# Kernel tuning notes

Measured on AMD Instinct MI355X. Metric: run time of the kernel, lower is better.

Reference implementation:

```python
import jax, jax.numpy as jnp
import numpy as np

N, E, K, D, H, ED = 10000, 200000, 16, 64, 4, 16


def setup_inputs() -> dict:
    key = jax.random.key(0)
    ks = iter(jax.random.split(key, 64))
    def nrm(shape, s=1.0):
        return jax.random.normal(next(ks), shape, dtype=jnp.float32) * s
    def lin(fi, fo):
        return nrm((fi, fo), 1.0 / np.sqrt(fi))
    inp = {}
    inp['h'] = nrm((N, D))
    inp['coord'] = nrm((N, 3))
    nv = nrm((N, 3)); inp['nvecs'] = nv / (jnp.linalg.norm(nv, axis=-1, keepdims=True) + 1e-8)
    inp['edge_attr'] = nrm((E, ED))
    inp['node_attr'] = nrm((N, D))
    inp['init_coord'] = nrm((N, 3))
    iv = nrm((N, 3)); inp['init_nvecs'] = iv / (jnp.linalg.norm(iv, axis=-1, keepdims=True) + 1e-8)
    # Ch_Pos_GCL params (Linear weights stored as (in, out))
    inp['ch_W1'] = lin(4 * D + ED, D); inp['ch_b1'] = jnp.zeros((D,))
    inp['ch_W2'] = lin(D, D);          inp['ch_b2'] = jnp.zeros((D,))
    inp['pos_W1'] = lin(2, D);         inp['pos_b1'] = jnp.zeros((D,))
    inp['pos_W2'] = lin(D, D);         inp['pos_b2'] = jnp.zeros((D,))
    inp['sh_W'] = lin(D, D);           inp['sh_b'] = jnp.zeros((D,))
    inp['att_W'] = lin(D, 1);          inp['att_b'] = jnp.zeros((1,))
    # Tri_Att_GCL per-head params stacked over heads
    inp['Wq'] = nrm((H, D, D), 1.0 / np.sqrt(D))
    inp['Wk'] = nrm((H, D, D), 1.0 / np.sqrt(D))
    inp['Wv'] = nrm((H, D, D), 1.0 / np.sqrt(D))
    inp['Wb'] = nrm((H, D), 1.0 / np.sqrt(D))
    inp['Wg'] = nrm((H, D, D), 1.0 / np.sqrt(D))
    inp['bg'] = jnp.zeros((H, D))
    inp['out_W'] = lin(H * D, D);      inp['out_b'] = jnp.zeros((D,))
    # phi MLPs
    inp['phiu_W1'] = lin(D, D); inp['phiu_b1'] = jnp.zeros((D,)); inp['phiu_W2'] = lin(D, 1); inp['phiu_b2'] = jnp.zeros((1,))
    inp['phix_W1'] = lin(D, D); inp['phix_b1'] = jnp.zeros((D,)); inp['phix_W2'] = lin(D, 1); inp['phix_b2'] = jnp.zeros((1,))
    inp['phin_W1'] = lin(D, D); inp['phin_b1'] = jnp.zeros((D,)); inp['phin_W2'] = lin(D, 1); inp['phin_b2'] = jnp.zeros((1,))
    inp['phih_W1'] = lin(2 * D + D, D); inp['phih_b1'] = jnp.zeros((D,))
    inp['phih_W2'] = lin(D, D);         inp['phih_b2'] = jnp.zeros((D,))
    # int inputs
    inp['edges'] = jax.random.randint(next(ks), (2, E), 0, N)
    idx = jax.random.randint(next(ks), (E, 2, K), 0, E)
    pad = jax.random.uniform(next(ks), (E, 1, K)) < 0.1
    inp['klist'] = jnp.where(pad, -1, idx)
    return inp


def reference(h, coord, nvecs, edge_attr, node_attr, init_coord, init_nvecs,
              ch_W1, ch_b1, ch_W2, ch_b2, pos_W1, pos_b1, pos_W2, pos_b2,
              sh_W, sh_b, att_W, att_b, Wq, Wk, Wv, Wb, Wg, bg, out_W, out_b,
              phiu_W1, phiu_b1, phiu_W2, phiu_b2, phix_W1, phix_b1, phix_W2, phix_b2,
              phin_W1, phin_b1, phin_W2, phin_b2, phih_W1, phih_b1, phih_W2, phih_b2,
              edges, klist):
    silu = jax.nn.silu
    row, col = edges[0], edges[1]
    # --- Ch_Pos_GCL ---
    diff = coord[row] - coord[col]                      # (E, 3)
    radial = jnp.sum(diff * diff, axis=1, keepdims=True)
    coord_diff = diff / (jnp.sqrt(radial) + 1e-8)
    nprod = jnp.sum(nvecs[row] * nvecs[col], axis=-1, keepdims=True)
    chem_in = jnp.concatenate([h[row], h[col], node_attr[row], node_attr[col], edge_attr], axis=1)
    chem = silu(silu(chem_in @ ch_W1 + ch_b1) @ ch_W2 + ch_b2)          # (E, D)
    pos = silu(silu(jnp.concatenate([nprod, radial], axis=1) @ pos_W1 + pos_b1) @ pos_W2 + pos_b2)
    out = silu(chem @ sh_W + sh_b) * pos
    z = out * jax.nn.sigmoid(out @ att_W + att_b)                        # (E, D)
    # --- Tri_Att_GCL (k-neighbor triangle attention) ---
    idx_i2k, idx_j2k = klist[:, 0], klist[:, 1]          # (E, K)
    fmask = (idx_i2k != -1).astype(z.dtype)              # redundant slots -> 0
    scale = 1.0 / np.sqrt(D)
    head_outs = []
    for hd in range(H):
        q = z @ Wq[hd]; k = z @ Wk[hd]; v = z @ Wv[hd]
        b = z @ Wb[hd]                                   # (E,)
        g = jax.nn.sigmoid(z @ Wg[hd] + bg[hd])
        tri_k = k[idx_i2k] * fmask[..., None]            # (E, K, D)
        tri_v = v[idx_i2k] * fmask[..., None]
        tri_b = b[idx_j2k] * fmask                       # (E, K)
        alpha = jax.nn.softmax(scale * jnp.einsum('ed,ekd->ek', q, tri_k) + tri_b, axis=1)
        head_outs.append(g * jnp.einsum('ek,ekd->ed', alpha, tri_v))
    m = jnp.concatenate(head_outs, axis=-1) @ out_W + out_b             # (E, D)
    # --- aggregation / updates ---
    def mlp2(x, W1, b1, W2, b2):
        return silu(x @ W1 + b1) @ W2 + b2
    def seg_mean(data, ids, n):
        s = jax.ops.segment_sum(data, ids, num_segments=n)
        c = jax.ops.segment_sum(jnp.ones_like(data), ids, num_segments=n)
        return s / jnp.clip(c, 1.0)
    n_nodes = coord.shape[0]
    phi_u = mlp2(chem, phiu_W1, phiu_b1, phiu_W2, phiu_b2)              # (E, 1)
    phi_x = mlp2(pos, phix_W1, phix_b1, phix_W2, phix_b2)
    phi_n = mlp2(pos, phin_W1, phin_b1, phin_W2, phin_b2)
    x_agg = seg_mean(coord_diff * (phi_u * phi_x), row, n_nodes)
    coord_new = 0.2 * init_coord + 0.8 * coord + x_agg
    n_agg = seg_mean(nvecs[col] * (phi_u * phi_n), row, n_nodes)
    nv = 0.2 * init_nvecs + 0.8 * nvecs + n_agg
    nv = nv / (jnp.linalg.norm(nv, axis=-1, keepdims=True) + 1e-8)
    m_agg = seg_mean(m, row, n_nodes)
    h_new = 0.2 * h + 0.8 * mlp2(jnp.concatenate([h, node_attr, m_agg], axis=-1), phih_W1, phih_b1, phih_W2, phih_b2)
    return (h_new, coord_new, nv)
```

## Files before the change

kernel.cpp:

```cpp
#include <hip/hip_runtime.h>

typedef unsigned short u16;
typedef unsigned int u32;
typedef __attribute__((ext_vector_type(8))) short s16x8;
typedef __attribute__((ext_vector_type(4))) float f32x4;

#define NN 10000
#define EE 200000
#define ES ((size_t)EE * 64)
#define NTILE 3125

#define DEVI __device__ __forceinline__

DEVI float us2f(u16 u) {
    union { u32 i; float f; } v; v.i = ((u32)u) << 16; return v.f;
}
DEVI u16 f2bu(float f) {
    union { float f; u32 i; } v; v.f = f;
    u32 x = v.i;
    return (u16)((x + 0x7fffu + ((x >> 16) & 1u)) >> 16);
}
DEVI float siluf(float x) { return x / (1.f + __expf(-x)); }
DEVI float sigmf(float x) { return 1.f / (1.f + __expf(-x)); }
DEVI float waveSum(float v) {
#pragma unroll
    for (int o = 32; o; o >>= 1) v += __shfl_xor(v, o);
    return v;
}
DEVI float quadSum(float v) {
#pragma unroll
    for (int o = 1; o < 16; o <<= 1) v += __shfl_xor(v, o);
    return v;
}

__device__ u16 g_hb[(size_t)NN * 64];
__device__ u16 g_nab[(size_t)NN * 64];
__device__ u16 g_eab[(size_t)EE * 16];
__device__ u16 g_t1[ES];
__device__ u16 g_z16[ES];
__device__ u16 g_t4[4][ES];
__device__ __align__(16) u16 g_Mt[4][4608];
__device__ __align__(16) u16 g_wpre[12][4608];
__device__ __align__(16) u16 g_wmA[6][4608];
__device__ __align__(16) u16 g_w1t[64 * 296];
__device__ float g_b4[(size_t)EE * 4];
__device__ float g_nr[EE];
__device__ float g_rad[EE];
__device__ float g_cdl[EE * 3];
__device__ int g_degi[NN];
__device__ int g_fill[NN];
__device__ int g_roff[NN + 1];
__device__ int g_eid[EE];
__device__ float g_me[(size_t)EE * 64];
__device__ float g_xe[EE * 3];
__device__ float g_ne[EE * 3];
__device__ float g_mavg[(size_t)NN * 64];

__global__ __launch_bounds__(256) void k_zero()
{
    int t = blockIdx.x * 256 + threadIdx.x;
    if (t < NN) { g_degi[t] = 0; g_fill[t] = 0; }
}

__global__ __launch_bounds__(256) void k_prep(
    const float* __restrict__ Wq, const float* __restrict__ Wk,
    const float* __restrict__ h, const float* __restrict__ na, const float* __restrict__ ea,
    const float* __restrict__ coord, const float* __restrict__ nvecs,
    const float* __restrict__ Wv, const float* __restrict__ Wg, const float* __restrict__ oW,
    const float* __restrict__ posW2, const float* __restrict__ chW2, const float* __restrict__ shW,
    const float* __restrict__ uW1, const float* __restrict__ xW1, const float* __restrict__ nW1,
    const float* __restrict__ chemW1,
    const int* __restrict__ edges)
{
    int t = blockIdx.x * 256 + threadIdx.x;
    if (t < 16384) {
        int hd = t >> 12, rem = t & 4095, k = rem >> 6, n = rem & 63;
        const float* wq = Wq + (size_t)hd * 4096 + k * 64;
        const float* wk = Wk + (size_t)hd * 4096 + n * 64;
        float acc = 0.f;
        for (int d = 0; d < 64; d++) acc += wq[d] * wk[d];
        int off = n * 72 + k;
        g_Mt[hd][off] = f2bu(acc);
        g_wpre[hd * 3 + 0][off] = f2bu(Wv[t]);
        g_wpre[hd * 3 + 1][off] = f2bu(oW[t]);
        g_wpre[hd * 3 + 2][off] = f2bu(Wg[t]);
    }
    int nt = gridDim.x * 256;
    for (int i = t; i < 6 * 4096; i += nt) {
        int a = i >> 12, rem = i & 4095, k = rem >> 6, n = rem & 63;
        const float* s;
        if (a == 0) s = posW2;
        else if (a == 1) s = chW2;
        else if (a == 2) s = shW;
        else if (a == 3) s = uW1;
        else if (a == 4) s = xW1;
        else s = nW1;
        g_wmA[a][n * 72 + k] = f2bu(s[rem]);
    }
    for (int i = t; i < 64 * 296; i += nt) {
        int n = i / 296, k = i - n * 296;
        g_w1t[i] = (k < 272) ? f2bu(chemW1[k * 64 + n]) : (u16)0;
    }
    for (int i = t; i < NN * 64; i += nt) { g_hb[i] = f2bu(h[i]); g_nab[i] = f2bu(na[i]); }
    for (size_t i = t; i < (size_t)EE * 16; i += nt) g_eab[i] = f2bu(ea[i]);
    for (int e = t; e < EE; e += nt) {
        int r = edges[e], c = edges[EE + e];
        atomicAdd(&g_degi[r], 1);
        float d0 = coord[r * 3 + 0] - coord[c * 3 + 0];
        float d1 = coord[r * 3 + 1] - coord[c * 3 + 1];
        float d2 = coord[r * 3 + 2] - coord[c * 3 + 2];
        float radial = d0 * d0 + d1 * d1 + d2 * d2;
        float np = nvecs[r * 3 + 0] * nvecs[c * 3 + 0]
                 + nvecs[r * 3 + 1] * nvecs[c * 3 + 1]
                 + nvecs[r * 3 + 2] * nvecs[c * 3 + 2];
        float rinv = 1.f / (sqrtf(radial) + 1e-8f);
        g_cdl[e * 3 + 0] = d0 * rinv;
        g_cdl[e * 3 + 1] = d1 * rinv;
        g_cdl[e * 3 + 2] = d2 * rinv;
        g_nr[e] = np;
        g_rad[e] = radial;
    }
}

__global__ __launch_bounds__(256) void k_scan()
{
    __shared__ int ls[256];
    int tid = threadIdx.x;
    int basei = tid * 40;
    int loc[40];
    int cnt = 0;
#pragma unroll
    for (int i = 0; i < 40; i++) {
        int idx = basei + i;
        int v = (idx < NN) ? g_degi[idx] : 0;
        loc[i] = cnt; cnt += v;
    }
    ls[tid] = cnt;
    __syncthreads();
    int off = 0;
    for (int i = 0; i < tid; i++) off += ls[i];
#pragma unroll
    for (int i = 0; i < 40; i++) {
        int idx = basei + i;
        if (idx < NN) g_roff[idx] = off + loc[i];
    }
    if (tid == 255) g_roff[NN] = off + cnt;
}

__global__ __launch_bounds__(256) void k_fill(const int* __restrict__ edges)
{
    int e = blockIdx.x * 256 + threadIdx.x;
    if (e < EE) {
        int r = edges[e];
        int slot = atomicAdd(&g_fill[r], 1);
        g_eid[g_roff[r] + slot] = e;
    }
}

__global__ __launch_bounds__(256) void k_chem1(
    const int* __restrict__ edges, const float* __restrict__ b1)
{
    __shared__ __align__(16) u16 sBT[64 * 296];
    int tid = threadIdx.x;
    {
        u32* d = (u32*)sBT; const u32* s = (const u32*)g_w1t;
        for (int i = tid; i < 9472; i += 256) d[i] = s[i];
    }
    __syncthreads();
    int lane = tid & 63, q = lane >> 4, ln = lane & 15, w = tid >> 6;
    int base = blockIdx.x * 2;
    int nt2 = (base + 1 < NTILE) ? 2 : 1;
    for (int t2 = 0; t2 < nt2; t2++) {
        int m0 = (base + t2) * 64 + w * 16;
        int e = m0 + ln;
        int r_ = edges[e], c_ = edges[EE + e];
        f32x4 acc[4];
#pragma unroll
        for (int t = 0; t < 4; t++) acc[t] = (f32x4){0.f, 0.f, 0.f, 0.f};
#pragma unroll
        for (int k0 = 0; k0 < 9; k0++) {
            int k = k0 * 32 + q * 8;
            const u16* p = nullptr;
            if (k < 64)       p = g_hb  + (size_t)r_ * 64 + k;
            else if (k < 128) p = g_hb  + (size_t)c_ * 64 + (k - 64);
            else if (k < 192) p = g_nab + (size_t)r_ * 64 + (k - 128);
            else if (k < 256) p = g_nab + (size_t)c_ * 64 + (k - 192);
            else if (k < 272) p = g_eab + (size_t)e * 16 + (k - 256);
            s16x8 af = p ? *(const s16x8*)p : (s16x8){0, 0, 0, 0, 0, 0, 0, 0};
#pragma unroll
            for (int t = 0; t < 4; t++) {
                s16x8 bf = *(const s16x8*)(&sBT[(t * 16 + ln) * 296 + k0 * 32 + q * 8]);
                acc[t] = __builtin_amdgcn_mfma_f32_16x16x32_bf16(af, bf, acc[t], 0, 0, 0);
            }
        }
#pragma unroll
        for (int t = 0; t < 4; t++) {
            float bv = b1[t * 16 + ln];
#pragma unroll
            for (int r = 0; r < 4; r++)
                g_t1[(size_t)(m0 + q * 4 + r) * 64 + t * 16 + ln] = f2bu(siluf(acc[t][r] + bv));
        }
    }
}

DEVI void stageP(u16* dst, const u16* src, int tid) {
    u32* d = (u32*)dst; const u32* s = (const u32*)src;
    for (int i = tid; i < 2304; i += 256) d[i] = s[i];
}

__global__ __launch_bounds__(256) void k_megaAB(
    const float* __restrict__ chb2,
    const float* __restrict__ pW1, const float* __restrict__ pb1,
    const float* __restrict__ posb2,
    const float* __restrict__ shb,
    const float* __restrict__ attW, const float* __restrict__ attb,
    const float* __restrict__ Wb,
    const float* __restrict__ ub1, const float* __restrict__ uW2, const float* __restrict__ ub2,
    const float* __restrict__ xb1, const float* __restrict__ xW2, const float* __restrict__ xb2,
    const float* __restrict__ nb1, const float* __restrict__ nW2, const float* __restrict__ nb2,
    const int* __restrict__ edges, const float* __restrict__ nvecs)
{
    __shared__ __align__(16) u16 sW0[64 * 72], sW1b[64 * 72], sW2b[64 * 72];
    __shared__ u16 T[4][16 * 72];
    __shared__ float sWB[256], sATT[64], sPW1[128], sPB1[64];
    int tid = threadIdx.x;
    stageP(sW0, g_wmA[0], tid); stageP(sW1b, g_wmA[1], tid); stageP(sW2b, g_wmA[2], tid);
    sWB[tid] = Wb[tid];
    if (tid < 128) sPW1[tid] = pW1[tid];
    if (tid < 64) { sATT[tid] = attW[tid]; sPB1[tid] = pb1[tid]; }
    __syncthreads();
    int lane = tid & 63, q = lane >> 4, ln = lane & 15, w = tid >> 6;
    int m0 = blockIdx.x * 64 + w * 16;
    float np_ = g_nr[m0 + ln], rad_ = g_rad[m0 + ln];
    s16x8 p1f0, p1f1;
#pragma unroll
    for (int j = 0; j < 8; j++) {
        int k = q * 8 + j;
        p1f0[j] = (short)f2bu(siluf(sPB1[k] + np_ * sPW1[k] + rad_ * sPW1[64 + k]));
        k += 32;
        p1f1[j] = (short)f2bu(siluf(sPB1[k] + np_ * sPW1[k] + rad_ * sPW1[64 + k]));
    }
    f32x4 pacc[4];
#pragma unroll
    for (int t = 0; t < 4; t++) {
        f32x4 a = (f32x4){0,0,0,0};
        a = __builtin_amdgcn_mfma_f32_16x16x32_bf16(p1f0, *(const s16x8*)(&sW0[(t * 16 + ln) * 72 + q * 8]), a, 0, 0, 0);
        a = __builtin_amdgcn_mfma_f32_16x16x32_bf16(p1f1, *(const s16x8*)(&sW0[(t * 16 + ln) * 72 + 32 + q * 8]), a, 0, 0, 0);
        pacc[t] = a;
    }
    float posD[4][4];
#pragma unroll
    for (int t = 0; t < 4; t++) {
        float pb = posb2[t * 16 + ln];
#pragma unroll
        for (int r = 0; r < 4; r++) posD[t][r] = siluf(pacc[t][r] + pb);
    }
    f32x4 cacc[4];
#pragma unroll
    for (int t = 0; t < 4; t++) cacc[t] = (f32x4){0,0,0,0};
    {
        const u16* ar = g_t1 + (size_t)(m0 + ln) * 64;
#pragma unroll
        for (int k0 = 0; k0 < 2; k0++) {
            s16x8 af = *(const s16x8*)(ar + k0 * 32 + q * 8);
#pragma unroll
            for (int t = 0; t < 4; t++) {
                s16x8 bf = *(const s16x8*)(&sW1b[(t * 16 + ln) * 72 + k0 * 32 + q * 8]);
                cacc[t] = __builtin_amdgcn_mfma_f32_16x16x32_bf16(af, bf, cacc[t], 0, 0, 0);
            }
        }
    }
#pragma unroll
    for (int t = 0; t < 4; t++) {
        float cb = chb2[t * 16 + ln];
#pragma unroll
        for (int r = 0; r < 4; r++)
            T[w][(q * 4 + r) * 72 + t * 16 + ln] = f2bu(siluf(cacc[t][r] + cb));
    }
    asm volatile("s_waitcnt lgkmcnt(0)" ::: "memory");
    s16x8 ca0 = *(const s16x8*)(&T[w][ln * 72 + q * 8]);
    s16x8 ca1 = *(const s16x8*)(&T[w][ln * 72 + 32 + q * 8]);
    f32x4 sacc[4];
#pragma unroll
    for (int t = 0; t < 4; t++) {
        f32x4 a = (f32x4){0,0,0,0};
        a = __builtin_amdgcn_mfma_f32_16x16x32_bf16(ca0, *(const s16x8*)(&sW2b[(t * 16 + ln) * 72 + q * 8]), a, 0, 0, 0);
        a = __builtin_amdgcn_mfma_f32_16x16x32_bf16(ca1, *(const s16x8*)(&sW2b[(t * 16 + ln) * 72 + 32 + q * 8]), a, 0, 0, 0);
        sacc[t] = a;
    }
    float zv[4][4];
    float part4[4] = {0.f, 0.f, 0.f, 0.f};
#pragma unroll
    for (int t = 0; t < 4; t++) {
        float sb = shb[t * 16 + ln];
        float aw = sATT[t * 16 + ln];
#pragma unroll
        for (int r = 0; r < 4; r++) {
            float o = siluf(sacc[t][r] + sb) * posD[t][r];
            zv[t][r] = o;
            part4[r] += o * aw;
        }
    }
    float ab = attb[0];
#pragma unroll
    for (int r = 0; r < 4; r++) {
        float sg = sigmf(quadSum(part4[r]) + ab);
        size_t row = m0 + q * 4 + r;
#pragma unroll
        for (int t = 0; t < 4; t++) {
            float z = zv[t][r] * sg;
            zv[t][r] = z;
            g_z16[row * 64 + t * 16 + ln] = f2bu(z);
        }
    }
#pragma unroll
    for (int hd = 0; hd < 4; hd++) {
#pragma unroll
        for (int r = 0; r < 4; r++) {
            float p = 0.f;
#pragma unroll
            for (int t = 0; t < 4; t++) p += zv[t][r] * sWB[hd * 64 + t * 16 + ln];
            p = quadSum(p);
            if (ln == hd) g_b4[(size_t)(m0 + q * 4 + r) * 4 + hd] = p;
        }
    }
#pragma unroll
    for (int t = 0; t < 4; t++)
#pragma unroll
        for (int r = 0; r < 4; r++)
            T[w][(q * 4 + r) * 72 + t * 16 + ln] = f2bu(posD[t][r]);
    asm volatile("s_waitcnt lgkmcnt(0)" ::: "memory");
    s16x8 pa0 = *(const s16x8*)(&T[w][ln * 72 + q * 8]);
    s16x8 pa1 = *(const s16x8*)(&T[w][ln * 72 + 32 + q * 8]);
    __syncthreads();
    stageP(sW0, g_wmA[3], tid); stageP(sW1b, g_wmA[4], tid); stageP(sW2b, g_wmA[5], tid);
    __syncthreads();
    f32x4 uacc[4];
#pragma unroll
    for (int t = 0; t < 4; t++) {
        f32x4 a = (f32x4){0,0,0,0};
        a = __builtin_amdgcn_mfma_f32_16x16x32_bf16(ca0, *(const s16x8*)(&sW0[(t * 16 + ln) * 72 + q * 8]), a, 0, 0, 0);
        a = __builtin_amdgcn_mfma_f32_16x16x32_bf16(ca1, *(const s16x8*)(&sW0[(t * 16 + ln) * 72 + 32 + q * 8]), a, 0, 0, 0);
        uacc[t] = a;
    }
    float up[4] = {0.f, 0.f, 0.f, 0.f};
#pragma unroll
    for (int t = 0; t < 4; t++) {
        float ub = ub1[t * 16 + ln];
        float w2 = uW2[t * 16 + ln];
#pragma unroll
        for (int r = 0; r < 4; r++) up[r] += siluf(uacc[t][r] + ub) * w2;
    }
    float ub2v = ub2[0];
    float pu[4];
#pragma unroll
    for (int r = 0; r < 4; r++) pu[r] = quadSum(up[r]) + ub2v;
    f32x4 xacc[4], nacc[4];
#pragma unroll
    for (int t = 0; t < 4; t++) {
        f32x4 a = (f32x4){0,0,0,0}, b = (f32x4){0,0,0,0};
        a = __builtin_amdgcn_mfma_f32_16x16x32_bf16(pa0, *(const s16x8*)(&sW1b[(t * 16 + ln) * 72 + q * 8]), a, 0, 0, 0);
        a = __builtin_amdgcn_mfma_f32_16x16x32_bf16(pa1, *(const s16x8*)(&sW1b[(t * 16 + ln) * 72 + 32 + q * 8]), a, 0, 0, 0);
        b = __builtin_amdgcn_mfma_f32_16x16x32_bf16(pa0, *(const s16x8*)(&sW2b[(t * 16 + ln) * 72 + q * 8]), b, 0, 0, 0);
        b = __builtin_amdgcn_mfma_f32_16x16x32_bf16(pa1, *(const s16x8*)(&sW2b[(t * 16 + ln) * 72 + 32 + q * 8]), b, 0, 0, 0);
        xacc[t] = a; nacc[t] = b;
    }
    float xp[4] = {0,0,0,0}, npv[4] = {0,0,0,0};
#pragma unroll
    for (int t = 0; t < 4; t++) {
        float xb = xb1[t * 16 + ln], nb = nb1[t * 16 + ln];
        float xw = xW2[t * 16 + ln], nw = nW2[t * 16 + ln];
#pragma unroll
        for (int r = 0; r < 4; r++) {
            xp[r] += siluf(xacc[t][r] + xb) * xw;
            npv[r] += siluf(nacc[t][r] + nb) * nw;
        }
    }
    float xb2v = xb2[0], nb2v = nb2[0];
#pragma unroll
    for (int r = 0; r < 4; r++) {
        float phix = quadSum(xp[r]) + xb2v;
        float phin = quadSum(npv[r]) + nb2v;
        int row = m0 + q * 4 + r;
        float tx = pu[r] * phix, tn = pu[r] * phin;
        int cc = edges[EE + row];
        if (ln < 3) {
            g_xe[row * 3 + ln] = g_cdl[row * 3 + ln] * tx;
            g_ne[row * 3 + ln] = nvecs[cc * 3 + ln] * tn;
        }
    }
}

struct STG { s16x8 za0, za1, qb0, qb1; f32x4 bv; };

__global__ __launch_bounds__(64) void k_attn2(const int* __restrict__ klist)
{
    __shared__ u16 sQP[16][256];
    __shared__ u16 zT[16 * 72];
    __shared__ __align__(16) float sA[4][16];
    int lane = threadIdx.x & 63, q = lane >> 4, ln = lane & 15;
    int m0 = blockIdx.x * 16;
    u16* zw = zT;

    {
        const u16* zr = g_z16 + (size_t)(m0 + ln) * 64;
        s16x8 af0 = *(const s16x8*)(zr + q * 8);
        s16x8 af1 = *(const s16x8*)(zr + 32 + q * 8);
#pragma unroll
        for (int hd = 0; hd < 4; hd++) {
            f32x4 aM[4];
#pragma unroll
            for (int t = 0; t < 4; t++) {
                f32x4 a = (f32x4){0,0,0,0};
                a = __builtin_amdgcn_mfma_f32_16x16x32_bf16(af0, *(const s16x8*)(&g_Mt[hd][(t * 16 + ln) * 72 + q * 8]), a, 0, 0, 0);
                a = __builtin_amdgcn_mfma_f32_16x16x32_bf16(af1, *(const s16x8*)(&g_Mt[hd][(t * 16 + ln) * 72 + 32 + q * 8]), a, 0, 0, 0);
                aM[t] = a;
            }
#pragma unroll
            for (int t = 0; t < 4; t++)
#pragma unroll
                for (int r = 0; r < 4; r++)
                    sQP[q * 4 + r][hd * 64 + t * 16 + ln] = f2bu(aM[t][r]);
        }
    }
    asm volatile("s_waitcnt lgkmcnt(0)" ::: "memory");

    auto ldkl = [&](int j) -> int {
        return (lane < 32) ? klist[(size_t)(m0 + j) * 32 + lane] : -1;
    };
    auto stage = [&](int kv, int j) -> STG {
        STG s;
        s.za0 = (s16x8){0,0,0,0,0,0,0,0}; s.za1 = (s16x8){0,0,0,0,0,0,0,0};
        s.qb0 = (s16x8){0,0,0,0,0,0,0,0}; s.qb1 = (s16x8){0,0,0,0,0,0,0,0};
        int ij = __shfl(kv, ln);
        if (ij >= 0) {
            const u16* zr = g_z16 + (size_t)ij * 64;
            s.za0 = *(const s16x8*)(zr + q * 8);
            s.za1 = *(const s16x8*)(zr + 32 + q * 8);
        }
        if (ln < 4) {
            s.qb0 = *(const s16x8*)(&sQP[j][ln * 64 + q * 8]);
            s.qb1 = *(const s16x8*)(&sQP[j][ln * 64 + 32 + q * 8]);
        }
        s.bv = (f32x4){0.f, 0.f, 0.f, 0.f};
#pragma unroll
        for (int r = 0; r < 4; r++) {
            int ijj = __shfl(kv, q * 4 + r);
            int jj = __shfl(kv, 16 + q * 4 + r);
            s.bv[r] = (ijj >= 0 && ln < 4) ? g_b4[(size_t)jj * 4 + ln] : 0.f;
        }
        return s;
    };

    int kvA = ldkl(0), kvB = ldkl(1), kvC = ldkl(2);
    STG s0 = stage(kvA, 0);
    STG s1 = stage(kvB, 1);
#pragma unroll 1
    for (int j = 0; j < 16; j++) {
        int kvD = (j + 3 < 16) ? ldkl(j + 3) : -1;
        STG s2;
        if (j + 2 < 16) s2 = stage(kvC, j + 2);
        else {
            s2.za0 = (s16x8){0,0,0,0,0,0,0,0}; s2.za1 = s2.za0;
            s2.qb0 = s2.za0; s2.qb1 = s2.za0;
            s2.bv = (f32x4){0.f, 0.f, 0.f, 0.f};
        }
        f32x4 sc = (f32x4){0.f, 0.f, 0.f, 0.f};
        sc = __builtin_amdgcn_mfma_f32_16x16x32_bf16(s0.za0, s0.qb0, sc, 0, 0, 0);
        sc = __builtin_amdgcn_mfma_f32_16x16x32_bf16(s0.za1, s0.qb1, sc, 0, 0, 0);
        *(s16x8*)(&zw[ln * 72 + q * 8]) = s0.za0;
        *(s16x8*)(&zw[ln * 72 + 32 + q * 8]) = s0.za1;
        float s[4];
#pragma unroll
        for (int r = 0; r < 4; r++) s[r] = 0.125f * sc[r] + s0.bv[r];
        float mx = fmaxf(fmaxf(s[0], s[1]), fmaxf(s[2], s[3]));
        mx = fmaxf(mx, __shfl_xor(mx, 16));
        mx = fmaxf(mx, __shfl_xor(mx, 32));
        float ex[4], ps = 0.f;
#pragma unroll
        for (int r = 0; r < 4; r++) { ex[r] = __expf(s[r] - mx); ps += ex[r]; }
        ps += __shfl_xor(ps, 16);
        ps += __shfl_xor(ps, 32);
        float inv = 1.f / ps;
        if (ln < 4)
            *(f32x4*)&sA[ln][q * 4] = (f32x4){ex[0] * inv, ex[1] * inv, ex[2] * inv, ex[3] * inv};
        asm volatile("s_waitcnt lgkmcnt(0)" ::: "memory");
        float t0 = 0.f, t1 = 0.f, t2 = 0.f, t3 = 0.f;
#pragma unroll
        for (int j4 = 0; j4 < 4; j4++) {
            f32x4 a0 = *(const f32x4*)&sA[0][j4 * 4];
            f32x4 a1 = *(const f32x4*)&sA[1][j4 * 4];
            f32x4 a2 = *(const f32x4*)&sA[2][j4 * 4];
            f32x4 a3 = *(const f32x4*)&sA[3][j4 * 4];
#pragma unroll
            for (int r = 0; r < 4; r++) {
                float zz = us2f(zw[(j4 * 4 + r) * 72 + lane]);
                t0 += a0[r] * zz; t1 += a1[r] * zz; t2 += a2[r] * zz; t3 += a3[r] * zz;
            }
        }
        size_t ob = (size_t)(m0 + j) * 64 + lane;
        g_t4[0][ob] = f2bu(t0);
        g_t4[1][ob] = f2bu(t1);
        g_t4[2][ob] = f2bu(t2);
        g_t4[3][ob] = f2bu(t3);
        kvA = kvB; kvB = kvC; kvC = kvD;
        s0 = s1; s1 = s2;
    }
}

__global__ __launch_bounds__(256) void k_us(
    const float* __restrict__ bg, const int* __restrict__ edges)
{
    __shared__ u16 sU[4][16 * 72];
    int tid = threadIdx.x;
    int lane = tid & 63, q = lane >> 4, ln = lane & 15, w = tid >> 6;
    int m0 = blockIdx.x * 64 + w * 16;
    const u16* zr = g_z16 + (size_t)(m0 + ln) * 64;
    s16x8 za[2];
    za[0] = *(const s16x8*)(zr + q * 8);
    za[1] = *(const s16x8*)(zr + 32 + q * 8);
    f32x4 macc[4];
#pragma unroll
    for (int t = 0; t < 4; t++) macc[t] = (f32x4){0,0,0,0};
    for (int hd = 0; hd < 4; hd++) {
        const u16* wV = g_wpre[hd * 3 + 0];
        const u16* wO = g_wpre[hd * 3 + 1];
        const u16* wG = g_wpre[hd * 3 + 2];
        f32x4 vacc[4], gacc[4];
#pragma unroll
        for (int t = 0; t < 4; t++) { vacc[t] = (f32x4){0,0,0,0}; gacc[t] = (f32x4){0,0,0,0}; }
        const u16* ar = &g_t4[hd][(size_t)(m0 + ln) * 64];
#pragma unroll
        for (int k0 = 0; k0 < 2; k0++) {
            s16x8 af = *(const s16x8*)(ar + k0 * 32 + q * 8);
#pragma unroll
            for (int t = 0; t < 4; t++) {
                vacc[t] = __builtin_amdgcn_mfma_f32_16x16x32_bf16(
                    af, *(const s16x8*)(&wV[(t * 16 + ln) * 72 + k0 * 32 + q * 8]), vacc[t], 0, 0, 0);
                gacc[t] = __builtin_amdgcn_mfma_f32_16x16x32_bf16(
                    za[k0], *(const s16x8*)(&wG[(t * 16 + ln) * 72 + k0 * 32 + q * 8]), gacc[t], 0, 0, 0);
            }
        }
#pragma unroll
        for (int t = 0; t < 4; t++) {
            float bb = bg[hd * 64 + t * 16 + ln];
#pragma unroll
            for (int r = 0; r < 4; r++) {
                float u = vacc[t][r] * sigmf(gacc[t][r] + bb);
                sU[w][(q * 4 + r) * 72 + t * 16 + ln] = f2bu(u);
            }
        }
        asm volatile("s_waitcnt lgkmcnt(0)" ::: "memory");
#pragma unroll
        for (int k0 = 0; k0 < 2; k0++) {
            s16x8 af = *(const s16x8*)(&sU[w][ln * 72 + k0 * 32 + q * 8]);
#pragma unroll
            for (int t = 0; t < 4; t++) {
                macc[t] = __builtin_amdgcn_mfma_f32_16x16x32_bf16(
                    af, *(const s16x8*)(&wO[(t * 16 + ln) * 72 + k0 * 32 + q * 8]), macc[t], 0, 0, 0);
            }
        }
        asm volatile("s_waitcnt lgkmcnt(0)" ::: "memory");
    }
#pragma unroll
    for (int r = 0; r < 4; r++) {
        size_t dst = (size_t)(m0 + q * 4 + r) * 64;
#pragma unroll
        for (int t = 0; t < 4; t++) g_me[dst + t * 16 + ln] = macc[t][r];
    }
}

__global__ __launch_bounds__(256) void k_agg(
    const float* __restrict__ coord, const float* __restrict__ nvecs,
    const float* __restrict__ icoord, const float* __restrict__ invecs,
    const float* __restrict__ ob, float* __restrict__ out)
{
    int tid = threadIdx.x;
    int lane = tid & 63;
    int n = blockIdx.x * 4 + (tid >> 6);
    if (n >= NN) return;
    int r0 = g_roff[n], r1 = g_roff[n + 1];
    int deg = r1 - r0;
    float msA = 0.f, msB = 0.f, msC = 0.f, msD = 0.f;
    float xs0 = 0.f, xs1 = 0.f, xs2 = 0.f, ns0 = 0.f, ns1 = 0.f, ns2 = 0.f;
    for (int base = r0; base < r1; base += 64) {
        int idx = base + lane;
        int e_l = (idx < r1) ? g_eid[idx] : -1;
        int cnt = min(64, r1 - base);
        int j = 0;
        for (; j + 3 < cnt; j += 4) {
            int ea = __shfl(e_l, j), eb = __shfl(e_l, j + 1);
            int ec = __shfl(e_l, j + 2), ed = __shfl(e_l, j + 3);
            msA += g_me[(size_t)ea * 64 + lane];
            msB += g_me[(size_t)eb * 64 + lane];
            msC += g_me[(size_t)ec * 64 + lane];
            msD += g_me[(size_t)ed * 64 + lane];
        }
        for (; j < cnt; j++) {
            int ea = __shfl(e_l, j);
            msA += g_me[(size_t)ea * 64 + lane];
        }
        if (e_l >= 0) {
            xs0 += g_xe[e_l * 3 + 0]; xs1 += g_xe[e_l * 3 + 1]; xs2 += g_xe[e_l * 3 + 2];
            ns0 += g_ne[e_l * 3 + 0]; ns1 += g_ne[e_l * 3 + 1]; ns2 += g_ne[e_l * 3 + 2];
        }
    }
    xs0 = waveSum(xs0); xs1 = waveSum(xs1); xs2 = waveSum(xs2);
    ns0 = waveSum(ns0); ns1 = waveSum(ns1); ns2 = waveSum(ns2);
    float rinv = 1.f / fmaxf((float)deg, 1.f);
    float obv = (deg > 0) ? ob[lane] : 0.f;
    g_mavg[(size_t)n * 64 + lane] = (msA + msB + msC + msD) * rinv + obv;
    if (lane == 0) {
        size_t coff = (size_t)NN * 64;
        size_t noff = coff + (size_t)NN * 3;
        float xs[3] = {xs0, xs1, xs2}, ns[3] = {ns0, ns1, ns2};
        float nl[3];
#pragma unroll
        for (int c = 0; c < 3; c++) {
            out[coff + n * 3 + c] = 0.2f * icoord[n * 3 + c] + 0.8f * coord[n * 3 + c] + xs[c] * rinv;
            nl[c] = 0.2f * invecs[n * 3 + c] + 0.8f * nvecs[n * 3 + c] + ns[c] * rinv;
        }
        float nn2 = sqrtf(nl[0] * nl[0] + nl[1] * nl[1] + nl[2] * nl[2]) + 1e-8f;
#pragma unroll
        for (int c = 0; c < 3; c++) out[noff + n * 3 + c] = nl[c] / nn2;
    }
}

__global__ __launch_bounds__(256) void k_node(
    const float* __restrict__ h, const float* __restrict__ na,
    const float* __restrict__ W1, const float* __restrict__ b1,
    const float* __restrict__ W2, const float* __restrict__ b2,
    float* __restrict__ out)
{
    __shared__ u16 sW1T[64 * 200];
    __shared__ u16 sW2T[64 * 72];
    __shared__ u16 sA[64 * 200];
    __shared__ u16 sT[64 * 72];
    __shared__ float sb2v[64];
    int tid = threadIdx.x;
    int m0 = blockIdx.x * 64;
    for (int i = tid; i < 64 * 192; i += 256) {
        int n = i / 192, k = i - n * 192;
        sW1T[n * 200 + k] = f2bu(W1[k * 64 + n]);
    }
    for (int i = tid; i < 4096; i += 256) {
        int k = i >> 6, n = i & 63;
        sW2T[n * 72 + k] = f2bu(W2[i]);
    }
    if (tid < 64) sb2v[tid] = b2[tid];
    for (int i = tid; i < 4096; i += 256) {
        int row = i >> 6, d = i & 63;
        int n = m0 + row; if (n >= NN) n = NN - 1;
        sA[row * 200 + d] = f2bu(h[(size_t)n * 64 + d]);
        sA[row * 200 + 64 + d] = f2bu(na[(size_t)n * 64 + d]);
        sA[row * 200 + 128 + d] = f2bu(g_mavg[(size_t)n * 64 + d]);
    }
    __syncthreads();
    int lane = tid & 63, q = lane >> 4, ln = lane & 15, w = tid >> 6;
    f32x4 acc[4];
#pragma unroll
    for (int t = 0; t < 4; t++) acc[t] = (f32x4){0.f, 0.f, 0.f, 0.f};
#pragma unroll
    for (int k0 = 0; k0 < 6; k0++) {
        s16x8 af = *(const s16x8*)(&sA[(w * 16 + ln) * 200 + k0 * 32 + q * 8]);
#pragma unroll
        for (int t = 0; t < 4; t++) {
            s16x8 bf = *(const s16x8*)(&sW1T[(t * 16 + ln) * 200 + k0 * 32 + q * 8]);
            acc[t] = __builtin_amdgcn_mfma_f32_16x16x32_bf16(af, bf, acc[t], 0, 0, 0);
        }
    }
#pragma unroll
    for (int t = 0; t < 4; t++) {
        float bv = b1[t * 16 + ln];
#pragma unroll
        for (int r = 0; r < 4; r++)
            sT[(w * 16 + q * 4 + r) * 72 + t * 16 + ln] = f2bu(siluf(acc[t][r] + bv));
    }
    asm volatile("s_waitcnt lgkmcnt(0)" ::: "memory");
    f32x4 acc2[4];
#pragma unroll
    for (int t = 0; t < 4; t++) acc2[t] = (f32x4){0.f, 0.f, 0.f, 0.f};
#pragma unroll
    for (int k0 = 0; k0 < 2; k0++) {
        s16x8 af = *(const s16x8*)(&sT[(w * 16 + ln) * 72 + k0 * 32 + q * 8]);
#pragma unroll
        for (int t = 0; t < 4; t++) {
            s16x8 bf = *(const s16x8*)(&sW2T[(t * 16 + ln) * 72 + k0 * 32 + q * 8]);
            acc2[t] = __builtin_amdgcn_mfma_f32_16x16x32_bf16(af, bf, acc2[t], 0, 0, 0);
        }
    }
#pragma unroll
    for (int r = 0; r < 4; r++) {
        int n = m0 + w * 16 + q * 4 + r;
        if (n < NN) {
#pragma unroll
            for (int t = 0; t < 4; t++) {
                int d = t * 16 + ln;
                out[(size_t)n * 64 + d] = 0.2f * h[(size_t)n * 64 + d] + 0.8f * (acc2[t][r] + sb2v[d]);
            }
        }
    }
}

extern "C" void kernel_launch(void* const* d_in, const int* in_sizes, int n_in,
                              void* d_out, int out_size, void* d_ws, size_t ws_size,
                              hipStream_t stream)
{
    const int* edges = (const int*)d_in[43];
    const int* klist = (const int*)d_in[44];
    auto F = [&](int i) { return (const float*)d_in[i]; };

    k_zero<<<40, 256, 0, stream>>>();
    k_prep<<<512, 256, 0, stream>>>(F(19), F(20), F(0), F(4), F(3), F(1), F(2),
                                    F(21), F(23), F(25),
                                    F(13), F(9), F(15), F(27), F(31), F(35), F(7),
                                    edges);
    k_scan<<<1, 256, 0, stream>>>();
    k_fill<<<782, 256, 0, stream>>>(edges);
    k_chem1<<<1563, 256, 0, stream>>>(edges, F(8));
    k_megaAB<<<3125, 256, 0, stream>>>(F(10), F(11), F(12), F(14),
                                       F(16), F(17), F(18), F(22),
                                       F(28), F(29), F(30),
                                       F(32), F(33), F(34),
                                       F(36), F(37), F(38),
                                       edges, F(2));
    k_attn2<<<12500, 64, 0, stream>>>(klist);
    k_us<<<3125, 256, 0, stream>>>(F(24), edges);
    k_agg<<<2500, 256, 0, stream>>>(F(1), F(2), F(5), F(6), F(26), (float*)d_out);
    k_node<<<157, 256, 0, stream>>>(F(0), F(4), F(39), F(40), F(41), F(42), (float*)d_out);
}
```

Measured before the change: 642.3 us.

## Fuse gated value/output projection into attention kernel, keep head outputs in LDS

The per-head attention results are now kept in shared memory inside the attention kernel, and the gated V projection plus output projection run in the same kernel instead of a separate launch. This removes writing and re-reading four E×64 bf16 intermediate arrays through global memory, plus one kernel launch. In exchange the attention kernel uses more LDS and registers, which may lower occupancy, and the projection now runs as 64-thread blocks instead of 256-thread blocks.

```diff
diff --git a/kernel.cpp b/kernel.cpp
--- a/kernel.cpp
+++ b/kernel.cpp
@@ -38,7 +38,6 @@
 __device__ u16 g_eab[(size_t)EE * 16];
 __device__ u16 g_t1[ES];
 __device__ u16 g_z16[ES];
-__device__ u16 g_t4[4][ES];
 __device__ __align__(16) u16 g_Mt[4][4608];
 __device__ __align__(16) u16 g_wpre[12][4608];
 __device__ __align__(16) u16 g_wmA[6][4608];
@@ -393,27 +392,29 @@
 
 struct STG { s16x8 za0, za1, qb0, qb1; f32x4 bv; };
 
-__global__ __launch_bounds__(64) void k_attn2(const int* __restrict__ klist)
-{
-    __shared__ u16 sQP[16][256];
-    __shared__ u16 zT[16 * 72];
+__global__ __launch_bounds__(64) void k_attn2(const int* __restrict__ klist,
+                                              const float* __restrict__ bg)
+{
+    __shared__ __align__(16) u16 sQP[16][256];
+    __shared__ __align__(16) u16 zT[16 * 72];
+    __shared__ __align__(16) u16 sT4[4][16 * 72];
     __shared__ __align__(16) float sA[4][16];
     int lane = threadIdx.x & 63, q = lane >> 4, ln = lane & 15;
     int m0 = blockIdx.x * 16;
     u16* zw = zT;
 
+    const u16* zro = g_z16 + (size_t)(m0 + ln) * 64;
+    s16x8 zaf0 = *(const s16x8*)(zro + q * 8);
+    s16x8 zaf1 = *(const s16x8*)(zro + 32 + q * 8);
     {
-        const u16* zr = g_z16 + (size_t)(m0 + ln) * 64;
-        s16x8 af0 = *(const s16x8*)(zr + q * 8);
-        s16x8 af1 = *(const s16x8*)(zr + 32 + q * 8);
 #pragma unroll
         for (int hd = 0; hd < 4; hd++) {
             f32x4 aM[4];
 #pragma unroll
             for (int t = 0; t < 4; t++) {
                 f32x4 a = (f32x4){0,0,0,0};
-                a = __builtin_amdgcn_mfma_f32_16x16x32_bf16(af0, *(const s16x8*)(&g_Mt[hd][(t * 16 + ln) * 72 + q * 8]), a, 0, 0, 0);
-                a = __builtin_amdgcn_mfma_f32_16x16x32_bf16(af1, *(const s16x8*)(&g_Mt[hd][(t * 16 + ln) * 72 + 32 + q * 8]), a, 0, 0, 0);
+                a = __builtin_amdgcn_mfma_f32_16x16x32_bf16(zaf0, *(const s16x8*)(&g_Mt[hd][(t * 16 + ln) * 72 + q * 8]), a, 0, 0, 0);
+                a = __builtin_amdgcn_mfma_f32_16x16x32_bf16(zaf1, *(const s16x8*)(&g_Mt[hd][(t * 16 + ln) * 72 + 32 + q * 8]), a, 0, 0, 0);
                 aM[t] = a;
             }
 #pragma unroll
@@ -498,27 +499,16 @@
                 t0 += a0[r] * zz; t1 += a1[r] * zz; t2 += a2[r] * zz; t3 += a3[r] * zz;
             }
         }
-        size_t ob = (size_t)(m0 + j) * 64 + lane;
-        g_t4[0][ob] = f2bu(t0);
-        g_t4[1][ob] = f2bu(t1);
-        g_t4[2][ob] = f2bu(t2);
-        g_t4[3][ob] = f2bu(t3);
+        sT4[0][j * 72 + lane] = f2bu(t0);
+        sT4[1][j * 72 + lane] = f2bu(t1);
+        sT4[2][j * 72 + lane] = f2bu(t2);
+        sT4[3][j * 72 + lane] = f2bu(t3);
         kvA = kvB; kvB = kvC; kvC = kvD;
         s0 = s1; s1 = s2;
     }
-}
-
-__global__ __launch_bounds__(256) void k_us(
-    const float* __restrict__ bg, const int* __restrict__ edges)
-{
-    __shared__ u16 sU[4][16 * 72];
-    int tid = threadIdx.x;
-    int lane = tid & 63, q = lane >> 4, ln = lane & 15, w = tid >> 6;
-    int m0 = blockIdx.x * 64 + w * 16;
-    const u16* zr = g_z16 + (size_t)(m0 + ln) * 64;
-    s16x8 za[2];
-    za[0] = *(const s16x8*)(zr + q * 8);
-    za[1] = *(const s16x8*)(zr + 32 + q * 8);
+
+    asm volatile("s_waitcnt lgkmcnt(0)" ::: "memory");
+    u16* uT = &sQP[0][0];
     f32x4 macc[4];
 #pragma unroll
     for (int t = 0; t < 4; t++) macc[t] = (f32x4){0,0,0,0};
@@ -529,16 +519,16 @@
         f32x4 vacc[4], gacc[4];
 #pragma unroll
         for (int t = 0; t < 4; t++) { vacc[t] = (f32x4){0,0,0,0}; gacc[t] = (f32x4){0,0,0,0}; }
-        const u16* ar = &g_t4[hd][(size_t)(m0 + ln) * 64];
 #pragma unroll
         for (int k0 = 0; k0 < 2; k0++) {
-            s16x8 af = *(const s16x8*)(ar + k0 * 32 + q * 8);
+            s16x8 af = *(const s16x8*)(&sT4[hd][ln * 72 + k0 * 32 + q * 8]);
+            s16x8 zf = (k0 == 0) ? zaf0 : zaf1;
 #pragma unroll
             for (int t = 0; t < 4; t++) {
                 vacc[t] = __builtin_amdgcn_mfma_f32_16x16x32_bf16(
                     af, *(const s16x8*)(&wV[(t * 16 + ln) * 72 + k0 * 32 + q * 8]), vacc[t], 0, 0, 0);
                 gacc[t] = __builtin_amdgcn_mfma_f32_16x16x32_bf16(
-                    za[k0], *(const s16x8*)(&wG[(t * 16 + ln) * 72 + k0 * 32 + q * 8]), gacc[t], 0, 0, 0);
+                    zf, *(const s16x8*)(&wG[(t * 16 + ln) * 72 + k0 * 32 + q * 8]), gacc[t], 0, 0, 0);
             }
         }
 #pragma unroll
@@ -547,13 +537,13 @@
 #pragma unroll
             for (int r = 0; r < 4; r++) {
                 float u = vacc[t][r] * sigmf(gacc[t][r] + bb);
-                sU[w][(q * 4 + r) * 72 + t * 16 + ln] = f2bu(u);
+                uT[(q * 4 + r) * 72 + t * 16 + ln] = f2bu(u);
             }
         }
         asm volatile("s_waitcnt lgkmcnt(0)" ::: "memory");
 #pragma unroll
         for (int k0 = 0; k0 < 2; k0++) {
-            s16x8 af = *(const s16x8*)(&sU[w][ln * 72 + k0 * 32 + q * 8]);
+            s16x8 af = *(const s16x8*)(&uT[ln * 72 + k0 * 32 + q * 8]);
 #pragma unroll
             for (int t = 0; t < 4; t++) {
                 macc[t] = __builtin_amdgcn_mfma_f32_16x16x32_bf16(
@@ -724,8 +714,7 @@
                                        F(32), F(33), F(34),
                                        F(36), F(37), F(38),
                                        edges, F(2));
-    k_attn2<<<12500, 64, 0, stream>>>(klist);
-    k_us<<<3125, 256, 0, stream>>>(F(24), edges);
+    k_attn2<<<12500, 64, 0, stream>>>(klist, F(24));
     k_agg<<<2500, 256, 0, stream>>>(F(1), F(2), F(5), F(6), F(26), (float*)d_out);
     k_node<<<157, 256, 0, stream>>>(F(0), F(4), F(39), F(40), F(41), F(42), (float*)d_out);
 }
```

Measured after the change: 609.6 us. 1.05x faster.
